# Performance work log

Measured on AMD Instinct MI355X. Metric: run time of the kernel, lower is better.

## Reference

```python
import jax, jax.numpy as jnp
import numpy as np

LN2 = 0.6931471805599453

def _logcosh(z):
    # numerically stable log(cosh(z)) = logaddexp(z, -z) - log(2)
    return jnp.logaddexp(z, -z) - LN2

def _logpsi(z, W, b, a):
    # RBM log-amplitude. z: [..., N] -> scalar per leading dims
    return z @ a + jnp.sum(_logcosh(z @ W + b), axis=-1)

def setup_inputs() -> dict:
    key = jax.random.key(0)
    k0, k1, k2, k3, k4 = jax.random.split(key, 5)
    B, N, H = 64, 512, 2048
    # spin configurations (sign pattern; flips y_k = x with site k negated work for any real values)
    x = jnp.sign(jax.random.normal(k0, (B, N), dtype=jnp.float32))
    # small init so exp(logpsi_y - logpsi_x) stays well-scaled
    W = 0.01 * jax.random.normal(k1, (N, H), dtype=jnp.float32)
    b = 0.01 * jax.random.normal(k2, (H,), dtype=jnp.float32)
    a = 0.01 * jax.random.normal(k3, (N,), dtype=jnp.float32)
    # per-connection operator matrix elements O(x, y_k)
    Oxy = jax.random.normal(k4, (N,), dtype=jnp.float32)
    return {"x": x, "W": W, "b": b, "a": a, "Oxy": Oxy}

def reference(x, W, b, a, Oxy):
    # eval_local_operator, vmapped over a batch of configurations.
    # operator.conn(x): y[k] = x with spin k flipped, with matrix element Oxy[k].
    B, N = x.shape
    flip = 1.0 - 2.0 * jnp.eye(N, dtype=x.dtype)          # [K=N, N]
    y = x[:, None, :] * flip[None, :, :]                  # [B, K, N] connected states
    logpsi_x = _logpsi(x, W, b, a)                        # [B]
    logpsi_y = _logpsi(y, W, b, a)                        # [B, K]
    # Oxy @ exp(logpsi_y - logpsi_x) per sample
    return jnp.einsum('k,bk->b', Oxy, jnp.exp(logpsi_y - logpsi_x[:, None]))
```

## Files before the change

### kernel.cpp

```cpp
#include <hip/hip_runtime.h>
#include <hip/hip_bf16.h>
#include <math.h>

constexpr int NB = 64;
constexpr int NN = 512;
constexpr int NH = 2048;
constexpr float LN2 = 0.6931471805599453f;

constexpr size_t OFF_T2 = 0;
constexpr size_t OFF_LC = OFF_T2 + (size_t)NN*NH;
constexpr size_t OFF_TT = OFF_LC + NN;

__global__ __launch_bounds__(512) void k_prep(const float* __restrict__ W,
                                              const float* __restrict__ x,
                                              const float* __restrict__ bvec,
                                              float* __restrict__ t2,
                                              float* __restrict__ LC,
                                              float* __restrict__ Tt,
                                              float* __restrict__ out) {
    __shared__ float sm[10240];
    int bid = blockIdx.x, tid = threadIdx.x;
    if (bid < NN) {
        int k = bid;
        const float4* wr = (const float4*)(W + (size_t)k * NH);
        float4* tr = (float4*)(t2 + (size_t)k * NH);
        float4 w0 = wr[tid];
        float in[4] = {w0.x, w0.y, w0.z, w0.w};
        float t[4], lsum = 0.f;
#pragma unroll
        for (int i = 0; i < 4; i++) {
            float y  = 2.0f * in[i];
            float ay = fabsf(y);
            float e  = __expf(-2.0f * ay);
            t[i] = copysignf((1.0f - e) / (1.0f + e), y);
            lsum += ay + __logf(1.0f + e) - LN2;
        }
        tr[tid] = make_float4(t[0], t[1], t[2], t[3]);
        sm[tid] = lsum; __syncthreads();
        for (int s = 256; s > 0; s >>= 1) {
            if (tid < s) sm[tid] += sm[tid + s];
            __syncthreads();
        }
        if (tid == 0) LC[k] = sm[0];
    } else {
        int gb = bid - NN;
        int ht = gb & 31;
        int bt = gb >> 5;
        {
            int j = tid >> 5, c = tid & 31;
            const float4* xr = (const float4*)(x + (size_t)(bt * 16 + j) * NN);
#pragma unroll
            for (int i = 0; i < 4; i++) {
                float4 v = xr[c + i * 32];
                int n0 = (c + i * 32) * 4;
                sm[(n0 + 0) * 20 + j] = v.x;
                sm[(n0 + 1) * 20 + j] = v.y;
                sm[(n0 + 2) * 20 + j] = v.z;
                sm[(n0 + 3) * 20 + j] = v.w;
            }
        }
        __syncthreads();
        int hl = tid & 63, ns = tid >> 6;
        int h  = ht * 64 + hl;
        float acc[16];
#pragma unroll
        for (int j = 0; j < 16; j++) acc[j] = 0.f;
        const float* wp = W + h;
#pragma unroll 4
        for (int n = ns * 64; n < ns * 64 + 64; n++) {
            float w = wp[(size_t)n * NH];
            const float4* xv = (const float4*)(sm + n * 20);
            float4 a0 = xv[0], a1 = xv[1], a2 = xv[2], a3 = xv[3];
            acc[0]  = fmaf(a0.x, w, acc[0]);  acc[1]  = fmaf(a0.y, w, acc[1]);
            acc[2]  = fmaf(a0.z, w, acc[2]);  acc[3]  = fmaf(a0.w, w, acc[3]);
            acc[4]  = fmaf(a1.x, w, acc[4]);  acc[5]  = fmaf(a1.y, w, acc[5]);
            acc[6]  = fmaf(a1.z, w, acc[6]);  acc[7]  = fmaf(a1.w, w, acc[7]);
            acc[8]  = fmaf(a2.x, w, acc[8]);  acc[9]  = fmaf(a2.y, w, acc[9]);
            acc[10] = fmaf(a2.z, w, acc[10]); acc[11] = fmaf(a2.w, w, acc[11]);
            acc[12] = fmaf(a3.x, w, acc[12]); acc[13] = fmaf(a3.y, w, acc[13]);
            acc[14] = fmaf(a3.z, w, acc[14]); acc[15] = fmaf(a3.w, w, acc[15]);
        }
        __syncthreads();
        float4* r4 = (float4*)sm;
#pragma unroll
        for (int q = 0; q < 4; q++)
            r4[(ns * 1024 + hl * 16) / 4 + q] =
                make_float4(acc[q*4], acc[q*4+1], acc[q*4+2], acc[q*4+3]);
        __syncthreads();
#pragma unroll
        for (int o = tid; o < 1024; o += 512) {
            int hl2 = o >> 4, j2 = o & 15;
            float th = bvec[ht * 64 + hl2];
#pragma unroll
            for (int n2 = 0; n2 < 8; n2++) th += sm[n2 * 1024 + hl2 * 16 + j2];
            float ay = fabsf(th);
            float e  = __expf(-2.0f * ay);
            Tt[(size_t)(ht * 64 + hl2) * NB + bt * 16 + j2] =
                copysignf((1.0f - e) / (1.0f + e), th);
        }
        if (gb == 0 && tid < NB) out[tid] = 0.f;
    }
}

__global__ __launch_bounds__(512) void k_main(const float* __restrict__ t2,
                                              const float* __restrict__ Tt,
                                              const float* __restrict__ x,
                                              const float* __restrict__ LC,
                                              const float* __restrict__ a,
                                              const float* __restrict__ Oxy,
                                              float* __restrict__ out) {
    __shared__ float red[8 * 2 * NB];
    int tid = threadIdx.x;
    int lane = tid & 63, wv = tid >> 6;
    int k0 = __builtin_amdgcn_readfirstlane(blockIdx.x * 2);
    float ms0 = -x[(size_t)lane * NN + k0];
    float ms1 = -x[(size_t)lane * NN + k0 + 1];
    const float* r0 = t2 + (size_t)k0 * NH;
    const float* r1 = r0 + NH;

    float lp0 = 0.f, lp1 = 0.f;
    int hb = wv * 256;
    for (int h0 = hb; h0 < hb + 256; h0 += 32) {
        float p0 = 1.f, p1 = 1.f;
#pragma unroll
        for (int hh = 0; hh < 32; hh++) {
            int h = h0 + hh;
            float T = Tt[(size_t)h * NB + lane];
            p0 *= fmaf(r0[h] * T, ms0, 1.0f);
            p1 *= fmaf(r1[h] * T, ms1, 1.0f);
        }
        lp0 += __logf(p0);
        lp1 += __logf(p1);
    }
    red[(wv * 2 + 0) * NB + lane] = lp0;
    red[(wv * 2 + 1) * NB + lane] = lp1;
    __syncthreads();
    if (tid < NB) {
        float d0 = LC[k0]     + 2.0f * ms0 * a[k0];
        float d1 = LC[k0 + 1] + 2.0f * ms1 * a[k0 + 1];
#pragma unroll
        for (int w2 = 0; w2 < 8; w2++) {
            d0 += red[(w2 * 2 + 0) * NB + tid];
            d1 += red[(w2 * 2 + 1) * NB + tid];
        }
        float c = Oxy[k0] * __expf(d0) + Oxy[k0 + 1] * __expf(d1);
        atomicAdd(&out[tid], c);
    }
}

extern "C" void kernel_launch(void* const* d_in, const int* in_sizes, int n_in,
                              void* d_out, int out_size, void* d_ws, size_t ws_size,
                              hipStream_t stream) {
    const float* x    = (const float*)d_in[0];
    const float* W    = (const float*)d_in[1];
    const float* bvec = (const float*)d_in[2];
    const float* a    = (const float*)d_in[3];
    const float* Oxy  = (const float*)d_in[4];
    float* out = (float*)d_out;

    float* ws = (float*)d_ws;
    float* t2 = ws + OFF_T2;
    float* LC = ws + OFF_LC;
    float* Tt = ws + OFF_TT;

    k_prep<<<NN + 128, 512, 0, stream>>>(W, x, bvec, t2, LC, Tt, out);
    k_main<<<NN / 2, 512, 0, stream>>>(t2, Tt, x, LC, a, Oxy, out);
}
```

Measured before the change: 94.13 us.

## Fuse tanh(2W) and logcosh row sums into main kernel via shared memory

Moves the per-row tanh(2W) and log-cosh sum computation out of the prep kernel and into k_main. Each block now computes its two W rows directly into shared memory, interleaved as pairs, and reduces the LC sum with wave shuffles. This removes the 4 MB t2 workspace write and reread and shrinks the prep grid to 128 theta blocks. The cost is extra transcendental work and a block barrier at the start of k_main.

```diff
diff --git a/kernel.cpp b/kernel.cpp
--- a/kernel.cpp
+++ b/kernel.cpp
@@ -7,127 +7,126 @@
 constexpr int NH = 2048;
 constexpr float LN2 = 0.6931471805599453f;
 
-constexpr size_t OFF_T2 = 0;
-constexpr size_t OFF_LC = OFF_T2 + (size_t)NN*NH;
-constexpr size_t OFF_TT = OFF_LC + NN;
+constexpr size_t OFF_TT = 0;
 
-__global__ __launch_bounds__(512) void k_prep(const float* __restrict__ W,
-                                              const float* __restrict__ x,
-                                              const float* __restrict__ bvec,
-                                              float* __restrict__ t2,
-                                              float* __restrict__ LC,
-                                              float* __restrict__ Tt,
-                                              float* __restrict__ out) {
+__global__ __launch_bounds__(512) void k_theta(const float* __restrict__ W,
+                                               const float* __restrict__ x,
+                                               const float* __restrict__ bvec,
+                                               float* __restrict__ Tt,
+                                               float* __restrict__ out) {
     __shared__ float sm[10240];
-    int bid = blockIdx.x, tid = threadIdx.x;
-    if (bid < NN) {
-        int k = bid;
-        const float4* wr = (const float4*)(W + (size_t)k * NH);
-        float4* tr = (float4*)(t2 + (size_t)k * NH);
-        float4 w0 = wr[tid];
-        float in[4] = {w0.x, w0.y, w0.z, w0.w};
-        float t[4], lsum = 0.f;
+    int tid = threadIdx.x;
+    int gb = blockIdx.x;
+    int ht = gb & 31;
+    int bt = gb >> 5;
+    {
+        int j = tid >> 5, c = tid & 31;
+        const float4* xr = (const float4*)(x + (size_t)(bt * 16 + j) * NN);
 #pragma unroll
         for (int i = 0; i < 4; i++) {
-            float y  = 2.0f * in[i];
-            float ay = fabsf(y);
-            float e  = __expf(-2.0f * ay);
-            t[i] = copysignf((1.0f - e) / (1.0f + e), y);
-            lsum += ay + __logf(1.0f + e) - LN2;
+            float4 v = xr[c + i * 32];
+            int n0 = (c + i * 32) * 4;
+            sm[(n0 + 0) * 20 + j] = v.x;
+            sm[(n0 + 1) * 20 + j] = v.y;
+            sm[(n0 + 2) * 20 + j] = v.z;
+            sm[(n0 + 3) * 20 + j] = v.w;
         }
-        tr[tid] = make_float4(t[0], t[1], t[2], t[3]);
-        sm[tid] = lsum; __syncthreads();
-        for (int s = 256; s > 0; s >>= 1) {
-            if (tid < s) sm[tid] += sm[tid + s];
-            __syncthreads();
-        }
-        if (tid == 0) LC[k] = sm[0];
-    } else {
-        int gb = bid - NN;
-        int ht = gb & 31;
-        int bt = gb >> 5;
-        {
-            int j = tid >> 5, c = tid & 31;
-            const float4* xr = (const float4*)(x + (size_t)(bt * 16 + j) * NN);
+    }
+    __syncthreads();
+    int hl = tid & 63, ns = tid >> 6;
+    int h  = ht * 64 + hl;
+    float acc[16];
 #pragma unroll
-            for (int i = 0; i < 4; i++) {
-                float4 v = xr[c + i * 32];
-                int n0 = (c + i * 32) * 4;
-                sm[(n0 + 0) * 20 + j] = v.x;
-                sm[(n0 + 1) * 20 + j] = v.y;
-                sm[(n0 + 2) * 20 + j] = v.z;
-                sm[(n0 + 3) * 20 + j] = v.w;
-            }
-        }
-        __syncthreads();
-        int hl = tid & 63, ns = tid >> 6;
-        int h  = ht * 64 + hl;
-        float acc[16];
+    for (int j = 0; j < 16; j++) acc[j] = 0.f;
+    const float* wp = W + h;
+#pragma unroll 4
+    for (int n = ns * 64; n < ns * 64 + 64; n++) {
+        float w = wp[(size_t)n * NH];
+        const float4* xv = (const float4*)(sm + n * 20);
+        float4 a0 = xv[0], a1 = xv[1], a2 = xv[2], a3 = xv[3];
+        acc[0]  = fmaf(a0.x, w, acc[0]);  acc[1]  = fmaf(a0.y, w, acc[1]);
+        acc[2]  = fmaf(a0.z, w, acc[2]);  acc[3]  = fmaf(a0.w, w, acc[3]);
+        acc[4]  = fmaf(a1.x, w, acc[4]);  acc[5]  = fmaf(a1.y, w, acc[5]);
+        acc[6]  = fmaf(a1.z, w, acc[6]);  acc[7]  = fmaf(a1.w, w, acc[7]);
+        acc[8]  = fmaf(a2.x, w, acc[8]);  acc[9]  = fmaf(a2.y, w, acc[9]);
+        acc[10] = fmaf(a2.z, w, acc[10]); acc[11] = fmaf(a2.w, w, acc[11]);
+        acc[12] = fmaf(a3.x, w, acc[12]); acc[13] = fmaf(a3.y, w, acc[13]);
+        acc[14] = fmaf(a3.z, w, acc[14]); acc[15] = fmaf(a3.w, w, acc[15]);
+    }
+    __syncthreads();
+    float4* r4 = (float4*)sm;
 #pragma unroll
-        for (int j = 0; j < 16; j++) acc[j] = 0.f;
-        const float* wp = W + h;
-#pragma unroll 4
-        for (int n = ns * 64; n < ns * 64 + 64; n++) {
-            float w = wp[(size_t)n * NH];
-            const float4* xv = (const float4*)(sm + n * 20);
-            float4 a0 = xv[0], a1 = xv[1], a2 = xv[2], a3 = xv[3];
-            acc[0]  = fmaf(a0.x, w, acc[0]);  acc[1]  = fmaf(a0.y, w, acc[1]);
-            acc[2]  = fmaf(a0.z, w, acc[2]);  acc[3]  = fmaf(a0.w, w, acc[3]);
-            acc[4]  = fmaf(a1.x, w, acc[4]);  acc[5]  = fmaf(a1.y, w, acc[5]);
-            acc[6]  = fmaf(a1.z, w, acc[6]);  acc[7]  = fmaf(a1.w, w, acc[7]);
-            acc[8]  = fmaf(a2.x, w, acc[8]);  acc[9]  = fmaf(a2.y, w, acc[9]);
-            acc[10] = fmaf(a2.z, w, acc[10]); acc[11] = fmaf(a2.w, w, acc[11]);
-            acc[12] = fmaf(a3.x, w, acc[12]); acc[13] = fmaf(a3.y, w, acc[13]);
-            acc[14] = fmaf(a3.z, w, acc[14]); acc[15] = fmaf(a3.w, w, acc[15]);
-        }
-        __syncthreads();
-        float4* r4 = (float4*)sm;
+    for (int q = 0; q < 4; q++)
+        r4[(ns * 1024 + hl * 16) / 4 + q] =
+            make_float4(acc[q*4], acc[q*4+1], acc[q*4+2], acc[q*4+3]);
+    __syncthreads();
 #pragma unroll
-        for (int q = 0; q < 4; q++)
-            r4[(ns * 1024 + hl * 16) / 4 + q] =
-                make_float4(acc[q*4], acc[q*4+1], acc[q*4+2], acc[q*4+3]);
-        __syncthreads();
+    for (int o = tid; o < 1024; o += 512) {
+        int hl2 = o >> 4, j2 = o & 15;
+        float th = bvec[ht * 64 + hl2];
 #pragma unroll
-        for (int o = tid; o < 1024; o += 512) {
-            int hl2 = o >> 4, j2 = o & 15;
-            float th = bvec[ht * 64 + hl2];
-#pragma unroll
-            for (int n2 = 0; n2 < 8; n2++) th += sm[n2 * 1024 + hl2 * 16 + j2];
-            float ay = fabsf(th);
-            float e  = __expf(-2.0f * ay);
-            Tt[(size_t)(ht * 64 + hl2) * NB + bt * 16 + j2] =
-                copysignf((1.0f - e) / (1.0f + e), th);
-        }
-        if (gb == 0 && tid < NB) out[tid] = 0.f;
+        for (int n2 = 0; n2 < 8; n2++) th += sm[n2 * 1024 + hl2 * 16 + j2];
+        float ay = fabsf(th);
+        float e  = __expf(-2.0f * ay);
+        Tt[(size_t)(ht * 64 + hl2) * NB + bt * 16 + j2] =
+            copysignf((1.0f - e) / (1.0f + e), th);
     }
+    if (gb == 0 && tid < NB) out[tid] = 0.f;
 }
 
-__global__ __launch_bounds__(512) void k_main(const float* __restrict__ t2,
+__global__ __launch_bounds__(512) void k_main(const float* __restrict__ W,
                                               const float* __restrict__ Tt,
                                               const float* __restrict__ x,
-                                              const float* __restrict__ LC,
                                               const float* __restrict__ a,
                                               const float* __restrict__ Oxy,
                                               float* __restrict__ out) {
-    __shared__ float red[8 * 2 * NB];
+    __shared__ float t2s[2 * NH];
+    __shared__ float red[16 * NB];
     int tid = threadIdx.x;
     int lane = tid & 63, wv = tid >> 6;
     int k0 = __builtin_amdgcn_readfirstlane(blockIdx.x * 2);
+    int hb = wv * 256;
+
+    const float2* w0 = (const float2*)(W + (size_t)k0 * NH + hb);
+    const float2* w1 = (const float2*)(W + (size_t)(k0 + 1) * NH + hb);
+    float lc0 = 0.f, lc1 = 0.f;
+#pragma unroll
+    for (int i = 0; i < 2; i++) {
+        float2 wa = w0[lane + i * 64];
+        float2 wb = w1[lane + i * 64];
+        float in[4] = {wa.x, wa.y, wb.x, wb.y};
+        float t[4];
+#pragma unroll
+        for (int j = 0; j < 4; j++) {
+            float y  = 2.0f * in[j];
+            float ay = fabsf(y);
+            float e  = __expf(-2.0f * ay);
+            t[j] = copysignf((1.0f - e) / (1.0f + e), y);
+            float l = ay + __logf(1.0f + e) - LN2;
+            if (j < 2) lc0 += l; else lc1 += l;
+        }
+        int h2 = hb + (lane + i * 64) * 2;
+        *(float4*)&t2s[h2 * 2] = make_float4(t[0], t[2], t[1], t[3]);
+    }
+#pragma unroll
+    for (int off = 32; off > 0; off >>= 1) {
+        lc0 += __shfl_xor(lc0, off);
+        lc1 += __shfl_xor(lc1, off);
+    }
     float ms0 = -x[(size_t)lane * NN + k0];
     float ms1 = -x[(size_t)lane * NN + k0 + 1];
-    const float* r0 = t2 + (size_t)k0 * NH;
-    const float* r1 = r0 + NH;
+    __syncthreads();
 
-    float lp0 = 0.f, lp1 = 0.f;
-    int hb = wv * 256;
+    float lp0 = lc0, lp1 = lc1;
     for (int h0 = hb; h0 < hb + 256; h0 += 32) {
         float p0 = 1.f, p1 = 1.f;
 #pragma unroll
         for (int hh = 0; hh < 32; hh++) {
             int h = h0 + hh;
+            float2 t = *(const float2*)&t2s[h * 2];
             float T = Tt[(size_t)h * NB + lane];
-            p0 *= fmaf(r0[h] * T, ms0, 1.0f);
-            p1 *= fmaf(r1[h] * T, ms1, 1.0f);
+            p0 *= fmaf(t.x * T, ms0, 1.0f);
+            p1 *= fmaf(t.y * T, ms1, 1.0f);
         }
         lp0 += __logf(p0);
         lp1 += __logf(p1);
@@ -136,8 +135,8 @@
     red[(wv * 2 + 1) * NB + lane] = lp1;
     __syncthreads();
     if (tid < NB) {
-        float d0 = LC[k0]     + 2.0f * ms0 * a[k0];
-        float d1 = LC[k0 + 1] + 2.0f * ms1 * a[k0 + 1];
+        float d0 = 2.0f * ms0 * a[k0];
+        float d1 = 2.0f * ms1 * a[k0 + 1];
 #pragma unroll
         for (int w2 = 0; w2 < 8; w2++) {
             d0 += red[(w2 * 2 + 0) * NB + tid];
@@ -158,11 +157,8 @@
     const float* Oxy  = (const float*)d_in[4];
     float* out = (float*)d_out;
 
-    float* ws = (float*)d_ws;
-    float* t2 = ws + OFF_T2;
-    float* LC = ws + OFF_LC;
-    float* Tt = ws + OFF_TT;
+    float* Tt = (float*)d_ws + OFF_TT;
 
-    k_prep<<<NN + 128, 512, 0, stream>>>(W, x, bvec, t2, LC, Tt, out);
-    k_main<<<NN / 2, 512, 0, stream>>>(t2, Tt, x, LC, a, Oxy, out);
+    k_theta<<<128, 512, 0, stream>>>(W, x, bvec, Tt, out);
+    k_main<<<NN / 2, 512, 0, stream>>>(W, Tt, x, a, Oxy, out);
 }
```

Result: faster. 90.39 us (-4.0%).
